# Kernel optimization log

Hardware: AMD Instinct MI355X
Metric: run time of the kernel (lower is better)

The kernel has to match this reference:

```python
import jax, jax.numpy as jnp
import numpy as np

N_NODES = 50000
N_EDGES = 800000
D_IN = 512
HIDDEN = 32
HEADS = 4
N_CLASSES = 40
NEG_SLOPE = 0.2


def gat_layer(x, W, a_src, a_dst, b, src, dst, num_nodes, concat):
    # x: [N, D], W: [D, H, C], a_src/a_dst: [H, C], b: [H*C] or [C]
    h = jnp.einsum('nd,dhc->nhc', x, W)  # [N, H, C]
    # attention logits per edge (edge j->i with j=src, i=dst)
    e = jnp.sum(h[src] * a_src, axis=-1) + jnp.sum(h[dst] * a_dst, axis=-1)  # [E, H]
    e = jnp.where(e > 0, e, NEG_SLOPE * e)  # leaky_relu
    # segment softmax over incoming edges of each dst node
    m = jax.ops.segment_max(e, dst, num_segments=num_nodes)  # [N, H]
    ex = jnp.exp(e - m[dst])
    denom = jax.ops.segment_sum(ex, dst, num_segments=num_nodes)
    alpha = ex / (denom[dst] + 1e-9)  # [E, H]
    # weighted scatter-aggregate of neighbor features
    out = jax.ops.segment_sum(alpha[:, :, None] * h[src], dst, num_segments=num_nodes)  # [N, H, C]
    if concat:
        out = out.reshape(num_nodes, -1)  # [N, H*C]
    else:
        out = out.mean(axis=1)  # [N, C]
    return out + b, alpha


def setup_inputs() -> dict:
    key = jax.random.key(0)
    ks = jax.random.split(key, 12)
    x = jax.random.normal(ks[0], (N_NODES, D_IN), dtype=jnp.float32)
    src = jax.random.randint(ks[1], (N_EDGES,), 0, N_NODES, dtype=jnp.int32)
    dst = jax.random.randint(ks[2], (N_EDGES,), 0, N_NODES, dtype=jnp.int32)
    s1 = 1.0 / np.sqrt(D_IN)
    W1 = jax.random.normal(ks[3], (D_IN, HEADS, HIDDEN), dtype=jnp.float32) * s1
    a_src1 = jax.random.normal(ks[4], (HEADS, HIDDEN), dtype=jnp.float32) * 0.1
    a_dst1 = jax.random.normal(ks[5], (HEADS, HIDDEN), dtype=jnp.float32) * 0.1
    b1 = jnp.zeros((HEADS * HIDDEN,), dtype=jnp.float32)
    d2 = HEADS * HIDDEN
    s2 = 1.0 / np.sqrt(d2)
    W2 = jax.random.normal(ks[6], (d2, 1, N_CLASSES), dtype=jnp.float32) * s2
    a_src2 = jax.random.normal(ks[7], (1, N_CLASSES), dtype=jnp.float32) * 0.1
    a_dst2 = jax.random.normal(ks[8], (1, N_CLASSES), dtype=jnp.float32) * 0.1
    b2 = jnp.zeros((N_CLASSES,), dtype=jnp.float32)
    return {"x": x, "src": src, "dst": dst,
            "W1": W1, "a_src1": a_src1, "a_dst1": a_dst1, "b1": b1,
            "W2": W2, "a_src2": a_src2, "a_dst2": a_dst2, "b2": b2}


def reference(x, src, dst, W1, a_src1, a_dst1, b1, W2, a_src2, a_dst2, b2):
    n = x.shape[0]
    # add self loops (standard in GATConv)
    loops = jnp.arange(n, dtype=src.dtype)
    s = jnp.concatenate([src, loops])
    d = jnp.concatenate([dst, loops])
    h1, _attn = gat_layer(x, W1, a_src1, a_dst1, b1, s, d, n, concat=True)
    h1 = jax.nn.elu(h1)
    h2, _ = gat_layer(h1, W2, a_src2, a_dst2, b2, s, d, n, concat=False)
    return jax.nn.softmax(h2, axis=-1)
```

## Files before the change

### kernel.cpp

```cpp
#include <hip/hip_runtime.h>
#include <hip/hip_bf16.h>
#include <math.h>

#define NN 50000
#define NE 800000
#define ET 850000
#define DIN 512
#define F1 128
#define NC 40
#define NEG 0.2f
#define CAP 128
#define SCAN_NB ((NN + 255) / 256)

typedef __attribute__((ext_vector_type(8))) short s16x8;
typedef __attribute__((ext_vector_type(4))) float f32x4;

__device__ inline unsigned short bfh(float f) {
    __hip_bfloat16 h = __float2bfloat16(f);
    return __builtin_bit_cast(unsigned short, h);
}
__device__ inline float bff(unsigned short u) {
    unsigned int x = (unsigned int)u << 16;
    return __builtin_bit_cast(float, x);
}

__device__ inline void split8(f32x4 v0, f32x4 v1, s16x8* hi, s16x8* lo) {
    float f[8] = {v0.x, v0.y, v0.z, v0.w, v1.x, v1.y, v1.z, v1.w};
    #pragma unroll
    for (int j = 0; j < 8; ++j) {
        unsigned short h = bfh(f[j]);
        (*hi)[j] = (short)h;
        (*lo)[j] = (short)bfh(f[j] - bff(h));
    }
}

__device__ inline void gl16(const void* g, void* l) {
    __builtin_amdgcn_global_load_lds((const __attribute__((address_space(1))) unsigned int*)g,
                                     (__attribute__((address_space(3))) unsigned int*)l, 16, 0, 0);
}

__global__ void prep_kernel(const float* __restrict__ W1,
        const float* __restrict__ W2, int* __restrict__ deg,
        unsigned short* __restrict__ Wh1T, unsigned short* __restrict__ Wl1T,
        unsigned short* __restrict__ Wh2T, unsigned short* __restrict__ Wl2T) {
    int i = blockIdx.x * blockDim.x + threadIdx.x;
    if (i < NN) deg[i] = 0;
    if (i < DIN * F1) {
        int k = i >> 7, c = i & 127;
        float w = W1[i];
        unsigned short h = bfh(w);
        unsigned short l = bfh(w - bff(h));
        Wh1T[c * DIN + k] = h;
        Wl1T[c * DIN + k] = l;
    }
    if (i < 48 * 128) {
        int c = i >> 7, k = i & 127;
        float w = (c < NC) ? W2[k * NC + c] : 0.f;
        unsigned short h = bfh(w);
        unsigned short l = bfh(w - bff(h));
        Wh2T[c * 128 + k] = h;
        Wl2T[c * 128 + k] = l;
    }
}

__global__ void hist_kernel(const int* __restrict__ dst, int* __restrict__ deg) {
    int e = blockIdx.x * blockDim.x + threadIdx.x;
    if (e >= ET) return;
    int d = (e < NE) ? dst[e] : (e - NE);
    atomicAdd(&deg[d], 1);
}

__global__ __launch_bounds__(256) void partial_kernel(const int* __restrict__ deg,
        int* __restrict__ bsum) {
    __shared__ int red[4];
    int i = blockIdx.x * 256 + threadIdx.x;
    int v = (i < NN) ? deg[i] : 0;
    #pragma unroll
    for (int o = 1; o < 64; o <<= 1) v += __shfl_xor(v, o);
    if ((threadIdx.x & 63) == 0) red[threadIdx.x >> 6] = v;
    __syncthreads();
    if (threadIdx.x == 0) bsum[blockIdx.x] = red[0] + red[1] + red[2] + red[3];
}

__global__ __launch_bounds__(256) void scanp_kernel(const int* __restrict__ bsum,
        int* __restrict__ bbase) {
    __shared__ int s[256];
    int t = threadIdx.x;
    s[t] = (t < SCAN_NB) ? bsum[t] : 0;
    __syncthreads();
    #pragma unroll
    for (int o = 1; o < 256; o <<= 1) {
        int v = (t >= o) ? s[t - o] : 0;
        __syncthreads();
        s[t] += v;
        __syncthreads();
    }
    if (t < SCAN_NB) bbase[t] = (t == 0) ? 0 : s[t - 1];
}

__global__ __launch_bounds__(256) void emit_kernel(const int* __restrict__ deg,
        const int* __restrict__ bbase, int* __restrict__ off, int* __restrict__ cur) {
    __shared__ int s[256];
    int t = threadIdx.x;
    int i = blockIdx.x * 256 + t;
    int d = (i < NN) ? deg[i] : 0;
    s[t] = d;
    __syncthreads();
    #pragma unroll
    for (int o = 1; o < 256; o <<= 1) {
        int v = (t >= o) ? s[t - o] : 0;
        __syncthreads();
        s[t] += v;
        __syncthreads();
    }
    int o0 = bbase[blockIdx.x] + s[t] - d;
    if (i < NN) { off[i] = o0; cur[i] = o0; }
    if (i == NN - 1) off[NN] = o0 + d;
}

__global__ void scatter_kernel(const int* __restrict__ src, const int* __restrict__ dst,
        int* __restrict__ cur, int* __restrict__ ssorted) {
    int e = blockIdx.x * blockDim.x + threadIdx.x;
    if (e >= ET) return;
    int s = (e < NE) ? src[e] : (e - NE);
    int d = (e < NE) ? dst[e] : (e - NE);
    int pos = atomicAdd(&cur[d], 1);
    ssorted[pos] = s;
}

__global__ __launch_bounds__(256) void gemm1_mfma(const float* __restrict__ X,
        const unsigned short* __restrict__ BhT, const unsigned short* __restrict__ BlT,
        const float* __restrict__ a_src, const float* __restrict__ a_dst,
        float* __restrict__ H, float* __restrict__ s1s, float* __restrict__ s1d) {
    __shared__ char lds[49152];
    char* ldsAh = lds;
    char* ldsAl = lds + 8192;
    char* ldsBh = lds + 16384;
    char* ldsBl = lds + 32768;
    const int tid = threadIdx.x;
    const int wid = tid >> 6, lane = tid & 63;
    const int wm = wid >> 1, wn = wid & 1;
    const int l15 = lane & 15, lg = lane >> 4;
    const int row0 = blockIdx.x * 64;

    const int arow = tid >> 2;
    const int akc  = (tid & 3) * 16;
    const int asw  = (arow & 7) << 4;
    int agr = row0 + arow; if (agr > NN - 1) agr = NN - 1;
    const float* aptr = X + (long)agr * DIN + akc;

    f32x4 acc[2][4];
    #pragma unroll
    for (int mi = 0; mi < 2; ++mi)
        #pragma unroll
        for (int ni = 0; ni < 4; ++ni) acc[mi][ni] = (f32x4)(0.f);

    for (int k0 = 0; k0 < DIN; k0 += 64) {
        #pragma unroll
        for (int p = 0; p < 4; ++p) {
            int q = p * 256 + tid;
            int dstoff = (p * 256 + wid * 64) << 4;
            int rr = q >> 3;
            int w = (q & 7) << 4;
            int sw = (rr & 7) << 4;
            long sb = (long)rr * (DIN * 2) + k0 * 2 + (w ^ sw);
            gl16((const char*)BhT + sb, ldsBh + dstoff);
            gl16((const char*)BlT + sb, ldsBl + dstoff);
        }
        {
            f32x4 v0 = *(const f32x4*)(aptr + k0);
            f32x4 v1 = *(const f32x4*)(aptr + k0 + 4);
            f32x4 v2 = *(const f32x4*)(aptr + k0 + 8);
            f32x4 v3 = *(const f32x4*)(aptr + k0 + 12);
            s16x8 h0, l0, h1, l1;
            split8(v0, v1, &h0, &l0);
            split8(v2, v3, &h1, &l1);
            int b0 = arow * 128 + ((akc * 2) ^ asw);
            int b1 = arow * 128 + ((akc * 2 + 16) ^ asw);
            *(s16x8*)(ldsAh + b0) = h0;
            *(s16x8*)(ldsAh + b1) = h1;
            *(s16x8*)(ldsAl + b0) = l0;
            *(s16x8*)(ldsAl + b1) = l1;
        }
        __syncthreads();
        #pragma unroll
        for (int ks = 0; ks < 2; ++ks) {
            s16x8 ah[2], al[2], bh[4], bl[4];
            #pragma unroll
            for (int mi = 0; mi < 2; ++mi) {
                int row = wm * 32 + mi * 16 + l15;
                int sw = (row & 7) << 4;
                int kb = (ks * 32 + lg * 8) * 2;
                ah[mi] = *(const s16x8*)(ldsAh + row * 128 + (kb ^ sw));
                al[mi] = *(const s16x8*)(ldsAl + row * 128 + (kb ^ sw));
            }
            #pragma unroll
            for (int ni = 0; ni < 4; ++ni) {
                int col = wn * 64 + ni * 16 + l15;
                int sw = (col & 7) << 4;
                int kb = (ks * 32 + lg * 8) * 2;
                bh[ni] = *(const s16x8*)(ldsBh + col * 128 + (kb ^ sw));
                bl[ni] = *(const s16x8*)(ldsBl + col * 128 + (kb ^ sw));
            }
            #pragma unroll
            for (int mi = 0; mi < 2; ++mi)
                #pragma unroll
                for (int ni = 0; ni < 4; ++ni) {
                    acc[mi][ni] = __builtin_amdgcn_mfma_f32_16x16x32_bf16(ah[mi], bh[ni], acc[mi][ni], 0, 0, 0);
                    acc[mi][ni] = __builtin_amdgcn_mfma_f32_16x16x32_bf16(ah[mi], bl[ni], acc[mi][ni], 0, 0, 0);
                    acc[mi][ni] = __builtin_amdgcn_mfma_f32_16x16x32_bf16(al[mi], bh[ni], acc[mi][ni], 0, 0, 0);
                }
        }
        __syncthreads();
    }

    #pragma unroll
    for (int mi = 0; mi < 2; ++mi)
        #pragma unroll
        for (int ni = 0; ni < 4; ++ni) {
            int col = wn * 64 + ni * 16 + l15;
            #pragma unroll
            for (int r = 0; r < 4; ++r) {
                int grow = row0 + wm * 32 + mi * 16 + lg * 4 + r;
                if (grow < NN) H[(long)grow * F1 + col] = acc[mi][ni][r];
            }
        }
    float av[4], bv[4];
    #pragma unroll
    for (int ni = 0; ni < 4; ++ni) {
        int col = wn * 64 + ni * 16 + l15;
        av[ni] = a_src[col];
        bv[ni] = a_dst[col];
    }
    #pragma unroll
    for (int mi = 0; mi < 2; ++mi)
        #pragma unroll
        for (int hl = 0; hl < 2; ++hl) {
            #pragma unroll
            for (int r = 0; r < 4; ++r) {
                float t1 = acc[mi][2 * hl][r] * av[2 * hl] + acc[mi][2 * hl + 1][r] * av[2 * hl + 1];
                float t2 = acc[mi][2 * hl][r] * bv[2 * hl] + acc[mi][2 * hl + 1][r] * bv[2 * hl + 1];
                #pragma unroll
                for (int o = 1; o < 16; o <<= 1) {
                    t1 += __shfl_xor(t1, o);
                    t2 += __shfl_xor(t2, o);
                }
                int grow = row0 + wm * 32 + mi * 16 + lg * 4 + r;
                if (l15 == 0 && grow < NN) {
                    int head = 2 * wn + hl;
                    s1s[grow * 4 + head] = t1;
                    s1d[grow * 4 + head] = t2;
                }
            }
        }
}

__global__ __launch_bounds__(256) void gemm2_mfma(const float* __restrict__ H1,
        const unsigned short* __restrict__ B2h, const unsigned short* __restrict__ B2l,
        const float* __restrict__ a_src, const float* __restrict__ a_dst,
        float* __restrict__ Z, float* __restrict__ s2s, float* __restrict__ s2d) {
    __shared__ char lds[57344];
    char* ldsA  = lds;
    char* ldsBh = lds + 32768;
    char* ldsBl = lds + 45056;
    const int tid = threadIdx.x;
    const int wid = tid >> 6, lane = tid & 63;
    const int l15 = lane & 15, lg = lane >> 4;
    const int row0 = blockIdx.x * 64;

    #pragma unroll
    for (int p = 0; p < 8; ++p) {
        int q = p * 256 + tid;
        int row = q >> 5;
        int w = (q & 31) << 4;
        int sw = (row & 7) << 4;
        int gr = row0 + row; if (gr > NN - 1) gr = NN - 1;
        gl16((const char*)(H1 + (long)gr * F1) + (w ^ sw), ldsA + ((p * 256 + wid * 64) << 4));
    }
    #pragma unroll
    for (int p = 0; p < 3; ++p) {
        int q = p * 256 + tid;
        int rr = q >> 4;
        int w = (q & 15) << 4;
        int sw = (rr & 7) << 4;
        int dstoff = (p * 256 + wid * 64) << 4;
        gl16((const char*)B2h + rr * 256 + (w ^ sw), ldsBh + dstoff);
        gl16((const char*)B2l + rr * 256 + (w ^ sw), ldsBl + dstoff);
    }
    __syncthreads();

    f32x4 acc[3];
    #pragma unroll
    for (int ni = 0; ni < 3; ++ni) acc[ni] = (f32x4)(0.f);

    #pragma unroll
    for (int ks = 0; ks < 4; ++ks) {
        int row = wid * 16 + l15;
        int sw = (row & 7) << 4;
        int kb = (ks * 32 + lg * 8) * 4;
        f32x4 v0 = *(const f32x4*)(ldsA + row * 512 + ((kb)      ^ sw));
        f32x4 v1 = *(const f32x4*)(ldsA + row * 512 + ((kb + 16) ^ sw));
        s16x8 ah, al;
        split8(v0, v1, &ah, &al);
        #pragma unroll
        for (int ni = 0; ni < 3; ++ni) {
            int cc = ni * 16 + l15;
            int swb = (cc & 7) << 4;
            int kb2 = (ks * 32 + lg * 8) * 2;
            s16x8 bh = *(const s16x8*)(ldsBh + cc * 256 + (kb2 ^ swb));
            s16x8 bl = *(const s16x8*)(ldsBl + cc * 256 + (kb2 ^ swb));
            acc[ni] = __builtin_amdgcn_mfma_f32_16x16x32_bf16(ah, bh, acc[ni], 0, 0, 0);
            acc[ni] = __builtin_amdgcn_mfma_f32_16x16x32_bf16(ah, bl, acc[ni], 0, 0, 0);
            acc[ni] = __builtin_amdgcn_mfma_f32_16x16x32_bf16(al, bh, acc[ni], 0, 0, 0);
        }
    }

    float av[3], bv[3];
    #pragma unroll
    for (int ni = 0; ni < 3; ++ni) {
        int cc = ni * 16 + l15;
        av[ni] = (cc < NC) ? a_src[cc] : 0.f;
        bv[ni] = (cc < NC) ? a_dst[cc] : 0.f;
    }
    #pragma unroll
    for (int r = 0; r < 4; ++r) {
        int grow = row0 + wid * 16 + lg * 4 + r;
        bool ok = grow < NN;
        float t1 = acc[0][r] * av[0] + acc[1][r] * av[1] + acc[2][r] * av[2];
        float t2 = acc[0][r] * bv[0] + acc[1][r] * bv[1] + acc[2][r] * bv[2];
        #pragma unroll
        for (int o = 1; o < 16; o <<= 1) {
            t1 += __shfl_xor(t1, o);
            t2 += __shfl_xor(t2, o);
        }
        #pragma unroll
        for (int ni = 0; ni < 3; ++ni) {
            int cc = ni * 16 + l15;
            if (ok && cc < NC) Z[(long)grow * NC + cc] = acc[ni][r];
        }
        if (ok && l15 == 0) { s2s[grow] = t1; s2d[grow] = t2; }
    }
}

__global__ __launch_bounds__(256) void fusedagg1_kernel(
        const int* __restrict__ off, const int* __restrict__ ssorted,
        const float* __restrict__ ssrc, const float* __restrict__ sdst,
        const float* __restrict__ H, const float* __restrict__ b,
        float* __restrict__ O) {
    __shared__ int idx_lds[4][CAP];
    __shared__ __align__(16) float e_lds[4][CAP][4];
    const int nd = threadIdx.x >> 6;
    int n = blockIdx.x * 4 + nd;
    if (n >= NN) return;
    const int lane = threadIdx.x & 63;
    const int base = off[n];
    const int deg  = off[n + 1] - base;
    const float4 vd = *(const float4*)(sdst + (long)n * 4);

    float m0 = -1e30f, m1 = -1e30f, m2 = -1e30f, m3 = -1e30f;
    for (int k = lane; k < deg; k += 64) {
        int s = ssorted[base + k];
        float4 vs = *(const float4*)(ssrc + (long)s * 4);
        float x0 = vs.x + vd.x; x0 = (x0 > 0.f) ? x0 : NEG * x0;
        float x1 = vs.y + vd.y; x1 = (x1 > 0.f) ? x1 : NEG * x1;
        float x2 = vs.z + vd.z; x2 = (x2 > 0.f) ? x2 : NEG * x2;
        float x3 = vs.w + vd.w; x3 = (x3 > 0.f) ? x3 : NEG * x3;
        if (k < CAP) {
            idx_lds[nd][k] = s;
            *(f32x4*)&e_lds[nd][k][0] = (f32x4){x0, x1, x2, x3};
        }
        m0 = fmaxf(m0, x0); m1 = fmaxf(m1, x1);
        m2 = fmaxf(m2, x2); m3 = fmaxf(m3, x3);
    }
    #pragma unroll
    for (int o = 1; o < 64; o <<= 1) {
        m0 = fmaxf(m0, __shfl_xor(m0, o));
        m1 = fmaxf(m1, __shfl_xor(m1, o));
        m2 = fmaxf(m2, __shfl_xor(m2, o));
        m3 = fmaxf(m3, __shfl_xor(m3, o));
    }
    float t0 = 0.f, t1 = 0.f, t2 = 0.f, t3 = 0.f;
    for (int k = lane; k < deg; k += 64) {
        float x0, x1, x2, x3;
        if (k < CAP) {
            f32x4 v = *(const f32x4*)&e_lds[nd][k][0];
            x0 = v.x; x1 = v.y; x2 = v.z; x3 = v.w;
        } else {
            int s = ssorted[base + k];
            float4 vs = *(const float4*)(ssrc + (long)s * 4);
            x0 = vs.x + vd.x; x0 = (x0 > 0.f) ? x0 : NEG * x0;
            x1 = vs.y + vd.y; x1 = (x1 > 0.f) ? x1 : NEG * x1;
            x2 = vs.z + vd.z; x2 = (x2 > 0.f) ? x2 : NEG * x2;
            x3 = vs.w + vd.w; x3 = (x3 > 0.f) ? x3 : NEG * x3;
        }
        float e0 = __expf(x0 - m0), e1 = __expf(x1 - m1);
        float e2 = __expf(x2 - m2), e3 = __expf(x3 - m3);
        if (k < CAP) *(f32x4*)&e_lds[nd][k][0] = (f32x4){e0, e1, e2, e3};
        t0 += e0; t1 += e1; t2 += e2; t3 += e3;
    }
    #pragma unroll
    for (int o = 1; o < 64; o <<= 1) {
        t0 += __shfl_xor(t0, o); t1 += __shfl_xor(t1, o);
        t2 += __shfl_xor(t2, o); t3 += __shfl_xor(t3, o);
    }
    const int hd = lane >> 4;
    const float inv = 1.f / (((hd == 0) ? t0 : (hd == 1) ? t1 : (hd == 2) ? t2 : t3) + 1e-9f);
    const float mh  = (hd == 0) ? m0 : (hd == 1) ? m1 : (hd == 2) ? m2 : m3;
    const float vdh = (hd == 0) ? vd.x : (hd == 1) ? vd.y : (hd == 2) ? vd.z : vd.w;
    float acc0 = 0.f, acc1 = 0.f;
    const int kend = (deg < CAP) ? deg : CAP;
    for (int k = 0; k < kend; ++k) {
        int s = idx_lds[nd][k];
        float e = e_lds[nd][k][hd];
        float2 hv = *(const float2*)(H + (long)s * F1 + 2 * lane);
        acc0 += e * hv.x;
        acc1 += e * hv.y;
    }
    for (int k = CAP; k < deg; ++k) {
        int s = ssorted[base + k];
        float4 vs = *(const float4*)(ssrc + (long)s * 4);
        float x = ((hd == 0) ? vs.x : (hd == 1) ? vs.y : (hd == 2) ? vs.z : vs.w) + vdh;
        x = (x > 0.f) ? x : NEG * x;
        float e = __expf(x - mh);
        float2 hv = *(const float2*)(H + (long)s * F1 + 2 * lane);
        acc0 += e * hv.x;
        acc1 += e * hv.y;
    }
    float2 bb = *(const float2*)(b + 2 * lane);
    float v0 = acc0 * inv + bb.x;
    float v1 = acc1 * inv + bb.y;
    v0 = (v0 > 0.f) ? v0 : expm1f(v0);
    v1 = (v1 > 0.f) ? v1 : expm1f(v1);
    float2 ov = {v0, v1};
    *(float2*)(O + (long)n * F1 + 2 * lane) = ov;
}

__global__ __launch_bounds__(256) void fusedagg2_kernel(
        const int* __restrict__ off, const int* __restrict__ ssorted,
        const float* __restrict__ ssrc, const float* __restrict__ sdst,
        const float* __restrict__ Z, const float* __restrict__ b,
        float* __restrict__ out) {
    __shared__ int   idx_lds[4][CAP];
    __shared__ float e_lds[4][CAP];
    const int nd = threadIdx.x >> 6;
    int n = blockIdx.x * 4 + nd;
    if (n >= NN) return;
    const int lane = threadIdx.x & 63;
    const int base = off[n];
    const int deg  = off[n + 1] - base;
    const float sdn = sdst[n];

    float m = -1e30f;
    for (int k = lane; k < deg; k += 64) {
        int s = ssorted[base + k];
        float x = ssrc[s] + sdn;
        x = (x > 0.f) ? x : NEG * x;
        if (k < CAP) { idx_lds[nd][k] = s; e_lds[nd][k] = x; }
        m = fmaxf(m, x);
    }
    #pragma unroll
    for (int o = 1; o < 64; o <<= 1) m = fmaxf(m, __shfl_xor(m, o));
    float t = 0.f;
    for (int k = lane; k < deg; k += 64) {
        float x;
        if (k < CAP) x = e_lds[nd][k];
        else {
            int s = ssorted[base + k];
            x = ssrc[s] + sdn;
            x = (x > 0.f) ? x : NEG * x;
        }
        float e = __expf(x - m);
        if (k < CAP) e_lds[nd][k] = e;
        t += e;
    }
    #pragma unroll
    for (int o = 1; o < 64; o <<= 1) t += __shfl_xor(t, o);
    const float inv = 1.f / (t + 1e-9f);

    float acc = 0.f;
    const int kend = (deg < CAP) ? deg : CAP;
    const bool act = lane < NC;
    for (int k = 0; k < kend; ++k) {
        int s = idx_lds[nd][k];
        float e = e_lds[nd][k];
        if (act) acc += e * Z[(long)s * NC + lane];
    }
    for (int k = CAP; k < deg; ++k) {
        int s = ssorted[base + k];
        float x = ssrc[s] + sdn;
        x = (x > 0.f) ? x : NEG * x;
        float e = __expf(x - m);
        if (act) acc += e * Z[(long)s * NC + lane];
    }
    float v = act ? acc * inv + b[lane] : -1e30f;
    float mx = v;
    #pragma unroll
    for (int o = 32; o > 0; o >>= 1) mx = fmaxf(mx, __shfl_xor(mx, o));
    float e = act ? __expf(v - mx) : 0.f;
    float sum = e;
    #pragma unroll
    for (int o = 32; o > 0; o >>= 1) sum += __shfl_xor(sum, o);
    if (act) out[(long)n * NC + lane] = e / sum;
}

extern "C" void kernel_launch(void* const* d_in, const int* in_sizes, int n_in,
                              void* d_out, int out_size, void* d_ws, size_t ws_size,
                              hipStream_t stream) {
    const float* x      = (const float*)d_in[0];
    const int*   src    = (const int*)  d_in[1];
    const int*   dst    = (const int*)  d_in[2];
    const float* W1     = (const float*)d_in[3];
    const float* a_src1 = (const float*)d_in[4];
    const float* a_dst1 = (const float*)d_in[5];
    const float* b1     = (const float*)d_in[6];
    const float* W2     = (const float*)d_in[7];
    const float* a_src2 = (const float*)d_in[8];
    const float* a_dst2 = (const float*)d_in[9];
    const float* b2     = (const float*)d_in[10];
    float* out = (float*)d_out;

    float* ws   = (float*)d_ws;
    float* hpre = ws;
    float* s1s  = hpre + 6400000;
    float* s1d  = s1s + 200000;
    float* h1   = s1d + 200000;
    float* z2   = h1 + 6400000;
    float* s2s  = z2 + 2000000;
    float* s2d  = s2s + 50000;
    int*   deg     = (int*)(s2d + 50000);
    int*   off     = deg + 50000;
    int*   cur     = off + 50008;
    int*   ssorted = cur + 50000;
    int*   bsum    = ssorted + 850000;
    int*   bbase   = bsum + 256;
    unsigned short* Wh1T = (unsigned short*)(bbase + 256);
    unsigned short* Wl1T = Wh1T + 65536;
    unsigned short* Wh2T = Wl1T + 65536;
    unsigned short* Wl2T = Wh2T + 6144;

    prep_kernel<<<(DIN * F1 + 255) / 256, 256, 0, stream>>>(W1, W2, deg, Wh1T, Wl1T, Wh2T, Wl2T);

    hist_kernel<<<(ET + 255) / 256, 256, 0, stream>>>(dst, deg);
    partial_kernel<<<SCAN_NB, 256, 0, stream>>>(deg, bsum);
    scanp_kernel<<<1, 256, 0, stream>>>(bsum, bbase);
    emit_kernel<<<SCAN_NB, 256, 0, stream>>>(deg, bbase, off, cur);
    scatter_kernel<<<(ET + 255) / 256, 256, 0, stream>>>(src, dst, cur, ssorted);

    gemm1_mfma<<<(NN + 63) / 64, 256, 0, stream>>>(x, Wh1T, Wl1T, a_src1, a_dst1, hpre, s1s, s1d);
    fusedagg1_kernel<<<(NN + 3) / 4, 256, 0, stream>>>(off, ssorted, s1s, s1d, hpre, b1, h1);

    gemm2_mfma<<<(NN + 63) / 64, 256, 0, stream>>>(h1, Wh2T, Wl2T, a_src2, a_dst2, z2, s2s, s2d);
    fusedagg2_kernel<<<(NN + 3) / 4, 256, 0, stream>>>(off, ssorted, s2s, s2d, z2, b2, out);
}
```

Before: 429.7 us.

## Split GAT aggregation into alpha pass and feature-sliced aggregation kernels

The fused per-node softmax-plus-aggregate kernels are each split in two. A first kernel computes normalized edge attention weights and writes them to a global buffer. A second kernel aggregates neighbor features, with each node's features split into 8 slices across separate blocks and edges spread over lanes, reduced by shuffles. Layer 2 also gets a separate softmax kernel. The goal is more parallelism and fewer serial per-edge loops over full rows, at the cost of extra global traffic for alpha, extra launches, and repeated index and offset reads across slices.

```diff
diff --git a/kernel.cpp b/kernel.cpp
--- a/kernel.cpp
+++ b/kernel.cpp
@@ -342,12 +342,10 @@
     }
 }
 
-__global__ __launch_bounds__(256) void fusedagg1_kernel(
+__global__ __launch_bounds__(256) void alpha1_kernel(
         const int* __restrict__ off, const int* __restrict__ ssorted,
         const float* __restrict__ ssrc, const float* __restrict__ sdst,
-        const float* __restrict__ H, const float* __restrict__ b,
-        float* __restrict__ O) {
-    __shared__ int idx_lds[4][CAP];
+        float* __restrict__ alphaN) {
     __shared__ __align__(16) float e_lds[4][CAP][4];
     const int nd = threadIdx.x >> 6;
     int n = blockIdx.x * 4 + nd;
@@ -365,10 +363,7 @@
         float x1 = vs.y + vd.y; x1 = (x1 > 0.f) ? x1 : NEG * x1;
         float x2 = vs.z + vd.z; x2 = (x2 > 0.f) ? x2 : NEG * x2;
         float x3 = vs.w + vd.w; x3 = (x3 > 0.f) ? x3 : NEG * x3;
-        if (k < CAP) {
-            idx_lds[nd][k] = s;
-            *(f32x4*)&e_lds[nd][k][0] = (f32x4){x0, x1, x2, x3};
-        }
+        if (k < CAP) *(f32x4*)&e_lds[nd][k][0] = (f32x4){x0, x1, x2, x3};
         m0 = fmaxf(m0, x0); m1 = fmaxf(m1, x1);
         m2 = fmaxf(m2, x2); m3 = fmaxf(m3, x3);
     }
@@ -403,44 +398,71 @@
         t0 += __shfl_xor(t0, o); t1 += __shfl_xor(t1, o);
         t2 += __shfl_xor(t2, o); t3 += __shfl_xor(t3, o);
     }
-    const int hd = lane >> 4;
-    const float inv = 1.f / (((hd == 0) ? t0 : (hd == 1) ? t1 : (hd == 2) ? t2 : t3) + 1e-9f);
-    const float mh  = (hd == 0) ? m0 : (hd == 1) ? m1 : (hd == 2) ? m2 : m3;
-    const float vdh = (hd == 0) ? vd.x : (hd == 1) ? vd.y : (hd == 2) ? vd.z : vd.w;
-    float acc0 = 0.f, acc1 = 0.f;
-    const int kend = (deg < CAP) ? deg : CAP;
-    for (int k = 0; k < kend; ++k) {
-        int s = idx_lds[nd][k];
-        float e = e_lds[nd][k][hd];
-        float2 hv = *(const float2*)(H + (long)s * F1 + 2 * lane);
-        acc0 += e * hv.x;
-        acc1 += e * hv.y;
-    }
-    for (int k = CAP; k < deg; ++k) {
-        int s = ssorted[base + k];
-        float4 vs = *(const float4*)(ssrc + (long)s * 4);
-        float x = ((hd == 0) ? vs.x : (hd == 1) ? vs.y : (hd == 2) ? vs.z : vs.w) + vdh;
-        x = (x > 0.f) ? x : NEG * x;
-        float e = __expf(x - mh);
-        float2 hv = *(const float2*)(H + (long)s * F1 + 2 * lane);
-        acc0 += e * hv.x;
-        acc1 += e * hv.y;
-    }
-    float2 bb = *(const float2*)(b + 2 * lane);
-    float v0 = acc0 * inv + bb.x;
-    float v1 = acc1 * inv + bb.y;
-    v0 = (v0 > 0.f) ? v0 : expm1f(v0);
-    v1 = (v1 > 0.f) ? v1 : expm1f(v1);
-    float2 ov = {v0, v1};
-    *(float2*)(O + (long)n * F1 + 2 * lane) = ov;
-}
-
-__global__ __launch_bounds__(256) void fusedagg2_kernel(
+    const float i0 = 1.f / (t0 + 1e-9f);
+    const float i1 = 1.f / (t1 + 1e-9f);
+    const float i2 = 1.f / (t2 + 1e-9f);
+    const float i3 = 1.f / (t3 + 1e-9f);
+    for (int k = lane; k < deg; k += 64) {
+        f32x4 e;
+        if (k < CAP) e = *(const f32x4*)&e_lds[nd][k][0];
+        else {
+            int s = ssorted[base + k];
+            float4 vs = *(const float4*)(ssrc + (long)s * 4);
+            float x0 = vs.x + vd.x; x0 = (x0 > 0.f) ? x0 : NEG * x0;
+            float x1 = vs.y + vd.y; x1 = (x1 > 0.f) ? x1 : NEG * x1;
+            float x2 = vs.z + vd.z; x2 = (x2 > 0.f) ? x2 : NEG * x2;
+            float x3 = vs.w + vd.w; x3 = (x3 > 0.f) ? x3 : NEG * x3;
+            e = (f32x4){__expf(x0 - m0), __expf(x1 - m1), __expf(x2 - m2), __expf(x3 - m3)};
+        }
+        e.x *= i0; e.y *= i1; e.z *= i2; e.w *= i3;
+        *(f32x4*)(alphaN + (long)(base + k) * 4) = e;
+    }
+}
+
+__global__ __launch_bounds__(256) void agg1_kernel(
+        const int* __restrict__ off, const int* __restrict__ ssorted,
+        const float* __restrict__ alphaN, const float* __restrict__ H,
+        const float* __restrict__ b, float* __restrict__ O) {
+    const int slice = blockIdx.x & 7;
+    const int chunk = blockIdx.x >> 3;
+    const int n = chunk * 4 + (threadIdx.x >> 6);
+    if (n >= NN) return;
+    const int lane = threadIdx.x & 63;
+    const int eg = lane >> 2, f = lane & 3;
+    const int base = off[n];
+    const int deg  = off[n + 1] - base;
+    const int head = slice >> 1;
+    const int c0 = slice * 16 + f * 4;
+    f32x4 acc = (f32x4)(0.f);
+    for (int k = eg; k < deg; k += 16) {
+        int p = base + k;
+        int s = ssorted[p];
+        float a = alphaN[(long)p * 4 + head];
+        f32x4 hv = *(const f32x4*)(H + (long)s * F1 + c0);
+        acc += (f32x4)(a) * hv;
+    }
+    #pragma unroll
+    for (int o = 4; o < 64; o <<= 1) {
+        acc.x += __shfl_xor(acc.x, o);
+        acc.y += __shfl_xor(acc.y, o);
+        acc.z += __shfl_xor(acc.z, o);
+        acc.w += __shfl_xor(acc.w, o);
+    }
+    if (eg == 0) {
+        f32x4 bb = *(const f32x4*)(b + c0);
+        f32x4 v = acc + bb;
+        v.x = (v.x > 0.f) ? v.x : expm1f(v.x);
+        v.y = (v.y > 0.f) ? v.y : expm1f(v.y);
+        v.z = (v.z > 0.f) ? v.z : expm1f(v.z);
+        v.w = (v.w > 0.f) ? v.w : expm1f(v.w);
+        *(f32x4*)(O + (long)n * F1 + c0) = v;
+    }
+}
+
+__global__ __launch_bounds__(256) void alpha2_kernel(
         const int* __restrict__ off, const int* __restrict__ ssorted,
         const float* __restrict__ ssrc, const float* __restrict__ sdst,
-        const float* __restrict__ Z, const float* __restrict__ b,
-        float* __restrict__ out) {
-    __shared__ int   idx_lds[4][CAP];
+        float* __restrict__ alphaN2) {
     __shared__ float e_lds[4][CAP];
     const int nd = threadIdx.x >> 6;
     int n = blockIdx.x * 4 + nd;
@@ -455,7 +477,7 @@
         int s = ssorted[base + k];
         float x = ssrc[s] + sdn;
         x = (x > 0.f) ? x : NEG * x;
-        if (k < CAP) { idx_lds[nd][k] = s; e_lds[nd][k] = x; }
+        if (k < CAP) e_lds[nd][k] = x;
         m = fmaxf(m, x);
     }
     #pragma unroll
@@ -476,31 +498,71 @@
     #pragma unroll
     for (int o = 1; o < 64; o <<= 1) t += __shfl_xor(t, o);
     const float inv = 1.f / (t + 1e-9f);
-
-    float acc = 0.f;
-    const int kend = (deg < CAP) ? deg : CAP;
-    const bool act = lane < NC;
-    for (int k = 0; k < kend; ++k) {
-        int s = idx_lds[nd][k];
-        float e = e_lds[nd][k];
-        if (act) acc += e * Z[(long)s * NC + lane];
-    }
-    for (int k = CAP; k < deg; ++k) {
-        int s = ssorted[base + k];
-        float x = ssrc[s] + sdn;
-        x = (x > 0.f) ? x : NEG * x;
-        float e = __expf(x - m);
-        if (act) acc += e * Z[(long)s * NC + lane];
-    }
-    float v = act ? acc * inv + b[lane] : -1e30f;
+    for (int k = lane; k < deg; k += 64) {
+        float e;
+        if (k < CAP) e = e_lds[nd][k];
+        else {
+            int s = ssorted[base + k];
+            float x = ssrc[s] + sdn;
+            x = (x > 0.f) ? x : NEG * x;
+            e = __expf(x - m);
+        }
+        alphaN2[base + k] = e * inv;
+    }
+}
+
+__global__ __launch_bounds__(256) void agg2_kernel(
+        const int* __restrict__ off, const int* __restrict__ ssorted,
+        const float* __restrict__ alphaN2, const float* __restrict__ Z,
+        const float* __restrict__ b, float* __restrict__ O2) {
+    const int slice = blockIdx.x & 7;
+    const int chunk = blockIdx.x >> 3;
+    const int n = chunk * 4 + (threadIdx.x >> 6);
+    if (n >= NN) return;
+    const int lane = threadIdx.x & 63;
+    const int base = off[n];
+    const int deg  = off[n + 1] - base;
+    const int c0 = slice * 5;
+    float a0 = 0.f, a1 = 0.f, a2 = 0.f, a3 = 0.f, a4 = 0.f;
+    for (int k = lane; k < deg; k += 64) {
+        int p = base + k;
+        int s = ssorted[p];
+        float a = alphaN2[p];
+        const float* zp = Z + (long)s * NC + c0;
+        a0 += a * zp[0]; a1 += a * zp[1]; a2 += a * zp[2];
+        a3 += a * zp[3]; a4 += a * zp[4];
+    }
+    #pragma unroll
+    for (int o = 1; o < 64; o <<= 1) {
+        a0 += __shfl_xor(a0, o); a1 += __shfl_xor(a1, o);
+        a2 += __shfl_xor(a2, o); a3 += __shfl_xor(a3, o);
+        a4 += __shfl_xor(a4, o);
+    }
+    if (lane == 0) {
+        float* op = O2 + (long)n * NC + c0;
+        op[0] = a0 + b[c0 + 0];
+        op[1] = a1 + b[c0 + 1];
+        op[2] = a2 + b[c0 + 2];
+        op[3] = a3 + b[c0 + 3];
+        op[4] = a4 + b[c0 + 4];
+    }
+}
+
+__global__ __launch_bounds__(256) void softmax_kernel(const float* __restrict__ O2,
+        float* __restrict__ out) {
+    long gt = (long)blockIdx.x * blockDim.x + threadIdx.x;
+    long n = gt >> 6;
+    int lane = threadIdx.x & 63;
+    if (n >= NN) return;
+    float v = (lane < NC) ? O2[n * NC + lane] : -1e30f;
     float mx = v;
     #pragma unroll
     for (int o = 32; o > 0; o >>= 1) mx = fmaxf(mx, __shfl_xor(mx, o));
-    float e = act ? __expf(v - mx) : 0.f;
+    float e = (lane < NC) ? __expf(v - mx) : 0.f;
     float sum = e;
     #pragma unroll
     for (int o = 32; o > 0; o >>= 1) sum += __shfl_xor(sum, o);
-    if (act) out[(long)n * NC + lane] = e / sum;
+    if (lane < NC) out[n * NC + lane] = e / sum;
 }
 
 extern "C" void kernel_launch(void* const* d_in, const int* in_sizes, int n_in,
@@ -527,7 +589,10 @@
     float* z2   = h1 + 6400000;
     float* s2s  = z2 + 2000000;
     float* s2d  = s2s + 50000;
-    int*   deg     = (int*)(s2d + 50000);
+    float* alphaN1 = s2d + 50000;
+    float* out2    = hpre;
+    float* alphaN2 = alphaN1;
+    int*   deg     = (int*)(alphaN1 + 3400000);
     int*   off     = deg + 50000;
     int*   cur     = off + 50008;
     int*   ssorted = cur + 50000;
@@ -547,8 +612,11 @@
     scatter_kernel<<<(ET + 255) / 256, 256, 0, stream>>>(src, dst, cur, ssorted);
 
     gemm1_mfma<<<(NN + 63) / 64, 256, 0, stream>>>(x, Wh1T, Wl1T, a_src1, a_dst1, hpre, s1s, s1d);
-    fusedagg1_kernel<<<(NN + 3) / 4, 256, 0, stream>>>(off, ssorted, s1s, s1d, hpre, b1, h1);
+    alpha1_kernel<<<(NN + 3) / 4, 256, 0, stream>>>(off, ssorted, s1s, s1d, alphaN1);
+    agg1_kernel<<<((NN + 3) / 4) * 8, 256, 0, stream>>>(off, ssorted, alphaN1, hpre, b1, h1);
 
     gemm2_mfma<<<(NN + 63) / 64, 256, 0, stream>>>(h1, Wh2T, Wl2T, a_src2, a_dst2, z2, s2s, s2d);
-    fusedagg2_kernel<<<(NN + 3) / 4, 256, 0, stream>>>(off, ssorted, s2s, s2d, z2, b2, out);
-}
+    alpha2_kernel<<<(NN + 3) / 4, 256, 0, stream>>>(off, ssorted, s2s, s2d, alphaN2);
+    agg2_kernel<<<((NN + 3) / 4) * 8, 256, 0, stream>>>(off, ssorted, alphaN2, z2, b2, out2);
+    softmax_kernel<<<(int)(((long)NN * 64 + 255) / 256), 256, 0, stream>>>(out2, out);
+}
```

New measurement: 611.5 us. 1.42x slower.

## Split neighbor aggregation across lane groups with wider vector gathers

Applied to the files above, without the earlier changes.

Both aggregation kernels now spread a node's incoming edges across lane groups. Layer 1 uses 4 groups of 16 lanes that each load 8 floats per edge, and layer 2 uses 8 groups of 8 lanes that each handle 5 of the 40 classes. The partial sums are then combined with cross-group shuffles. The serial per-edge loop becomes a quarter or an eighth as long, more gather loads can be in flight at once, and layer 2 no longer leaves 24 of 64 lanes idle. The cost is extra shuffle reductions, more registers for the accumulators, and a final epilogue in which only one group does any work.

```diff
diff --git a/kernel.cpp b/kernel.cpp
--- a/kernel.cpp
+++ b/kernel.cpp
@@ -403,36 +403,60 @@
         t0 += __shfl_xor(t0, o); t1 += __shfl_xor(t1, o);
         t2 += __shfl_xor(t2, o); t3 += __shfl_xor(t3, o);
     }
-    const int hd = lane >> 4;
-    const float inv = 1.f / (((hd == 0) ? t0 : (hd == 1) ? t1 : (hd == 2) ? t2 : t3) + 1e-9f);
+    const int g = lane >> 4;
+    const int l = lane & 15;
+    const int hd = l >> 2;
     const float mh  = (hd == 0) ? m0 : (hd == 1) ? m1 : (hd == 2) ? m2 : m3;
+    const float th  = (hd == 0) ? t0 : (hd == 1) ? t1 : (hd == 2) ? t2 : t3;
+    const float ih  = 1.f / (th + 1e-9f);
     const float vdh = (hd == 0) ? vd.x : (hd == 1) ? vd.y : (hd == 2) ? vd.z : vd.w;
-    float acc0 = 0.f, acc1 = 0.f;
+    const int c0 = l * 8;
+    f32x4 accA = (f32x4)(0.f), accB = (f32x4)(0.f);
     const int kend = (deg < CAP) ? deg : CAP;
-    for (int k = 0; k < kend; ++k) {
+    for (int k = g; k < kend; k += 4) {
         int s = idx_lds[nd][k];
         float e = e_lds[nd][k][hd];
-        float2 hv = *(const float2*)(H + (long)s * F1 + 2 * lane);
-        acc0 += e * hv.x;
-        acc1 += e * hv.y;
-    }
-    for (int k = CAP; k < deg; ++k) {
+        const float* hp = H + (long)s * F1 + c0;
+        f32x4 h0 = *(const f32x4*)(hp);
+        f32x4 h1 = *(const f32x4*)(hp + 4);
+        accA += (f32x4)(e) * h0;
+        accB += (f32x4)(e) * h1;
+    }
+    for (int k = CAP + g; k < deg; k += 4) {
         int s = ssorted[base + k];
         float4 vs = *(const float4*)(ssrc + (long)s * 4);
         float x = ((hd == 0) ? vs.x : (hd == 1) ? vs.y : (hd == 2) ? vs.z : vs.w) + vdh;
         x = (x > 0.f) ? x : NEG * x;
         float e = __expf(x - mh);
-        float2 hv = *(const float2*)(H + (long)s * F1 + 2 * lane);
-        acc0 += e * hv.x;
-        acc1 += e * hv.y;
-    }
-    float2 bb = *(const float2*)(b + 2 * lane);
-    float v0 = acc0 * inv + bb.x;
-    float v1 = acc1 * inv + bb.y;
-    v0 = (v0 > 0.f) ? v0 : expm1f(v0);
-    v1 = (v1 > 0.f) ? v1 : expm1f(v1);
-    float2 ov = {v0, v1};
-    *(float2*)(O + (long)n * F1 + 2 * lane) = ov;
+        const float* hp = H + (long)s * F1 + c0;
+        f32x4 h0 = *(const f32x4*)(hp);
+        f32x4 h1 = *(const f32x4*)(hp + 4);
+        accA += (f32x4)(e) * h0;
+        accB += (f32x4)(e) * h1;
+    }
+    #pragma unroll
+    for (int o = 16; o < 64; o <<= 1) {
+        accA.x += __shfl_xor(accA.x, o); accA.y += __shfl_xor(accA.y, o);
+        accA.z += __shfl_xor(accA.z, o); accA.w += __shfl_xor(accA.w, o);
+        accB.x += __shfl_xor(accB.x, o); accB.y += __shfl_xor(accB.y, o);
+        accB.z += __shfl_xor(accB.z, o); accB.w += __shfl_xor(accB.w, o);
+    }
+    if (g == 0) {
+        f32x4 bbA = *(const f32x4*)(b + c0);
+        f32x4 bbB = *(const f32x4*)(b + c0 + 4);
+        f32x4 vA = accA * (f32x4)(ih) + bbA;
+        f32x4 vB = accB * (f32x4)(ih) + bbB;
+        vA.x = (vA.x > 0.f) ? vA.x : expm1f(vA.x);
+        vA.y = (vA.y > 0.f) ? vA.y : expm1f(vA.y);
+        vA.z = (vA.z > 0.f) ? vA.z : expm1f(vA.z);
+        vA.w = (vA.w > 0.f) ? vA.w : expm1f(vA.w);
+        vB.x = (vB.x > 0.f) ? vB.x : expm1f(vB.x);
+        vB.y = (vB.y > 0.f) ? vB.y : expm1f(vB.y);
+        vB.z = (vB.z > 0.f) ? vB.z : expm1f(vB.z);
+        vB.w = (vB.w > 0.f) ? vB.w : expm1f(vB.w);
+        *(f32x4*)(O + (long)n * F1 + c0)     = vA;
+        *(f32x4*)(O + (long)n * F1 + c0 + 4) = vB;
+    }
 }
 
 __global__ __launch_bounds__(256) void fusedagg2_kernel(
@@ -477,30 +501,52 @@
     for (int o = 1; o < 64; o <<= 1) t += __shfl_xor(t, o);
     const float inv = 1.f / (t + 1e-9f);
 
-    float acc = 0.f;
+    const int g = lane >> 3;
+    const int l = lane & 7;
+    const int c0 = l * 5;
+    float a0 = 0.f, a1 = 0.f, a2 = 0.f, a3 = 0.f, a4 = 0.f;
     const int kend = (deg < CAP) ? deg : CAP;
-    const bool act = lane < NC;
-    for (int k = 0; k < kend; ++k) {
+    for (int k = g; k < kend; k += 8) {
         int s = idx_lds[nd][k];
         float e = e_lds[nd][k];
-        if (act) acc += e * Z[(long)s * NC + lane];
-    }
-    for (int k = CAP; k < deg; ++k) {
+        const float* zp = Z + (long)s * NC + c0;
+        a0 += e * zp[0]; a1 += e * zp[1]; a2 += e * zp[2];
+        a3 += e * zp[3]; a4 += e * zp[4];
+    }
+    for (int k = CAP + g; k < deg; k += 8) {
         int s = ssorted[base + k];
         float x = ssrc[s] + sdn;
         x = (x > 0.f) ? x : NEG * x;
         float e = __expf(x - m);
-        if (act) acc += e * Z[(long)s * NC + lane];
-    }
-    float v = act ? acc * inv + b[lane] : -1e30f;
-    float mx = v;
-    #pragma unroll
-    for (int o = 32; o > 0; o >>= 1) mx = fmaxf(mx, __shfl_xor(mx, o));
-    float e = act ? __expf(v - mx) : 0.f;
-    float sum = e;
-    #pragma unroll
-    for (int o = 32; o > 0; o >>= 1) sum += __shfl_xor(sum, o);
-    if (act) out[(long)n * NC + lane] = e / sum;
+        const float* zp = Z + (long)s * NC + c0;
+        a0 += e * zp[0]; a1 += e * zp[1]; a2 += e * zp[2];
+        a3 += e * zp[3]; a4 += e * zp[4];
+    }
+    #pragma unroll
+    for (int o = 8; o < 64; o <<= 1) {
+        a0 += __shfl_xor(a0, o); a1 += __shfl_xor(a1, o);
+        a2 += __shfl_xor(a2, o); a3 += __shfl_xor(a3, o);
+        a4 += __shfl_xor(a4, o);
+    }
+    if (g == 0) {
+        float v0 = a0 * inv + b[c0 + 0];
+        float v1 = a1 * inv + b[c0 + 1];
+        float v2 = a2 * inv + b[c0 + 2];
+        float v3 = a3 * inv + b[c0 + 3];
+        float v4 = a4 * inv + b[c0 + 4];
+        float mx = fmaxf(fmaxf(fmaxf(v0, v1), fmaxf(v2, v3)), v4);
+        #pragma unroll
+        for (int o = 1; o < 8; o <<= 1) mx = fmaxf(mx, __shfl_xor(mx, o));
+        float e0 = __expf(v0 - mx), e1 = __expf(v1 - mx), e2 = __expf(v2 - mx);
+        float e3 = __expf(v3 - mx), e4 = __expf(v4 - mx);
+        float s = e0 + e1 + e2 + e3 + e4;
+        #pragma unroll
+        for (int o = 1; o < 8; o <<= 1) s += __shfl_xor(s, o);
+        float is = 1.f / s;
+        float* op = out + (long)n * NC + c0;
+        op[0] = e0 * is; op[1] = e1 * is; op[2] = e2 * is;
+        op[3] = e3 * is; op[4] = e4 * is;
+    }
 }
 
 extern "C" void kernel_launch(void* const* d_in, const int* in_sizes, int n_in,
```

Result: faster. 401.2 us (-6.6%).
